# Performance work log

Hardware: AMD Instinct MI355X
Metric: run time of the kernel (lower is better)

The kernel has to match this reference:

```python
import jax, jax.numpy as jnp
import numpy as np

N = 50000
E = 1600000
IN_C = 128
HID = 64
HEADS = 4
OUT_C = 64
NEG_SLOPE = 0.2


def gat_layer(x, src, dst, W, a_src, a_dst, b, heads, ch):
    # x: [N, F_in], W: [F_in, heads*ch], a_src/a_dst: [heads, ch], b: [heads*ch]
    n = x.shape[0]
    h = (x @ W).reshape(n, heads, ch)                       # [N, H, C]
    alpha_s = jnp.einsum('nhc,hc->nh', h, a_src)            # [N, H]
    alpha_d = jnp.einsum('nhc,hc->nh', h, a_dst)
    e = jax.nn.leaky_relu(alpha_s[src] + alpha_d[dst], NEG_SLOPE)  # [Et, H]
    # segment softmax over incoming edges of each dst node (self-loops guarantee non-empty)
    m = jax.ops.segment_max(e, dst, num_segments=n)
    ex = jnp.exp(e - m[dst])
    denom = jax.ops.segment_sum(ex, dst, num_segments=n)
    alpha = ex / (denom[dst] + 1e-16)                       # [Et, H]
    out = jax.ops.segment_sum(h[src] * alpha[:, :, None], dst, num_segments=n)  # [N,H,C]
    return out.reshape(n, heads * ch) + b


def setup_inputs() -> dict:
    key = jax.random.key(0)
    ks = jax.random.split(key, 10)
    x = jax.random.normal(ks[0], (N, IN_C), dtype=jnp.float32)
    edge_index = jax.random.randint(ks[1], (2, E), 0, N, dtype=jnp.int64)
    s = 0.1
    W1 = jax.random.normal(ks[2], (IN_C, HEADS * HID), dtype=jnp.float32) * s
    a_src1 = jax.random.normal(ks[3], (HEADS, HID), dtype=jnp.float32) * s
    a_dst1 = jax.random.normal(ks[4], (HEADS, HID), dtype=jnp.float32) * s
    b1 = jnp.zeros((HEADS * HID,), dtype=jnp.float32)
    W2 = jax.random.normal(ks[5], (HEADS * HID, OUT_C), dtype=jnp.float32) * s
    a_src2 = jax.random.normal(ks[6], (1, OUT_C), dtype=jnp.float32) * s
    a_dst2 = jax.random.normal(ks[7], (1, OUT_C), dtype=jnp.float32) * s
    b2 = jnp.zeros((OUT_C,), dtype=jnp.float32)
    return {"x": x, "edge_index": edge_index, "W1": W1, "a_src1": a_src1,
            "a_dst1": a_dst1, "b1": b1, "W2": W2, "a_src2": a_src2,
            "a_dst2": a_dst2, "b2": b2}


def reference(x, edge_index, W1, a_src1, a_dst1, b1, W2, a_src2, a_dst2, b2):
    # add self-loops (PyG GATConv default)
    loops = jnp.arange(N, dtype=edge_index.dtype)
    src = jnp.concatenate([edge_index[0], loops])
    dst = jnp.concatenate([edge_index[1], loops])
    h = gat_layer(x, src, dst, W1, a_src1, a_dst1, b1, HEADS, HID)
    h = jax.nn.relu(h)
    out = gat_layer(h, src, dst, W2, a_src2, a_dst2, b2, 1, OUT_C)
    return out
```

## Files before the change

### kernel.cpp

```cpp
#include <hip/hip_runtime.h>
#include <cstdint>
#include <cstddef>

#define IN_C 128
#define CAP 72

typedef _Float16 __attribute__((ext_vector_type(2))) half2v;
typedef _Float16 __attribute__((ext_vector_type(4))) half4v;
typedef _Float16 __attribute__((ext_vector_type(8))) f16x8;
typedef float    __attribute__((ext_vector_type(4))) f32x4;
typedef unsigned __attribute__((ext_vector_type(2))) u32x2;
typedef unsigned __attribute__((ext_vector_type(4))) u32x4;

static __device__ __forceinline__ float lrelu(float x) { return x > 0.f ? x : 0.2f * x; }

static __device__ __forceinline__ unsigned pack2h(float a, float b) {
  union { _Float16 h[2]; unsigned u; } c;
  c.h[0] = (_Float16)a; c.h[1] = (_Float16)b;
  return c.u;
}
static __device__ __forceinline__ half2v bc_h2(unsigned u) {
  union { unsigned u; half2v h; } c; c.u = u; return c.h;
}

#if __has_builtin(__builtin_amdgcn_fdot2)
static __device__ __forceinline__ float FDOT2(half2v a, half2v b, float c) {
  return __builtin_amdgcn_fdot2(a, b, c, false);
}
#else
static __device__ __forceinline__ float FDOT2(half2v a, half2v b, float c) {
  return c + (float)a.x * (float)b.x + (float)a.y * (float)b.y;
}
#endif

__global__ void k_scatter_cnt(const int* __restrict__ ei_src, const int* __restrict__ ei_dst,
                              int* __restrict__ cnt, u32x2* __restrict__ sd,
                              int E, int Et, int nPerReg, int n) {
  int r = blockIdx.x & 7;
  int base = (blockIdx.x >> 3) * 1024 + threadIdx.x;
  int lo = r * nPerReg;
  int hi = lo + nPerReg; if (hi > n) hi = n;
#pragma unroll
  for (int k = 0; k < 4; ++k) {
    int e = base + k * 256;
    if (e >= Et) continue;
    int d = (e < E) ? __builtin_nontemporal_load(&ei_dst[e]) : (e - E);
    if (d < lo || d >= hi) continue;
    int s = (e < E) ? __builtin_nontemporal_load(&ei_src[e]) : d;
    int pos = atomicAdd(&cnt[d], 1);
    if (pos < CAP) {
      u32x2 rec = {(unsigned)s, (unsigned)d};
      sd[(size_t)d * CAP + pos] = rec;
    }
  }
}

__global__ void k_edgew(const u32x2* __restrict__ sd, const int* __restrict__ cnt,
                        const float* __restrict__ as1, const float* __restrict__ ad1,
                        u32x4* __restrict__ recs, int total) {
  int i = blockIdx.x * 256 + threadIdx.x;
  if (i >= total) return;
  int node = (int)((unsigned)i / CAP);
  int slot = i - node * CAP;
  int c = cnt[node]; if (c > CAP) c = CAP;
  if (slot >= c) return;
  u32x2 p = sd[i];
  float4 a = *(const float4*)&as1[p.x * 4];
  float4 b = *(const float4*)&ad1[p.y * 4];
  unsigned w01 = pack2h(__expf(lrelu(a.x + b.x)), __expf(lrelu(a.y + b.y)));
  unsigned w23 = pack2h(__expf(lrelu(a.z + b.z)), __expf(lrelu(a.w + b.w)));
  u32x4 rec = {p.x, w01, w23, p.y};
  recs[i] = rec;
}

__global__ void k_prep(const float* __restrict__ x, const float* __restrict__ W1,
                       const float* __restrict__ W2, const float* __restrict__ as_,
                       const float* __restrict__ ad_, _Float16* __restrict__ xh,
                       _Float16* __restrict__ W1t, _Float16* __restrict__ W2t,
                       float* __restrict__ V, int n4, int xb, int wb) {
  int b = blockIdx.x;
  if (b < xb) {
    int i = b * 256 + threadIdx.x;
    if (i >= n4) return;
    f32x4 v = __builtin_nontemporal_load((const f32x4*)&x[i * 4]);
    half4v o;
    o.x = (_Float16)v.x; o.y = (_Float16)v.y; o.z = (_Float16)v.z; o.w = (_Float16)v.w;
    *(half4v*)&xh[i * 4] = o;
  } else if (b < xb + wb) {
    int i = (b - xb) * 256 + threadIdx.x;
    if (i < 128 * 256) {
      int k = i / 256, nn = i % 256;
      W1t[(size_t)nn * 128 + k] = (_Float16)W1[i];
    } else {
      int j = i - 128 * 256;
      if (j < 256 * 64) {
        int k = j / 64, nn = j % 64;
        W2t[(size_t)nn * 256 + k] = (_Float16)W2[j];
      }
    }
  } else {
    int t = (b - xb - wb) * 256 + threadIdx.x;
    if (t >= 1024) return;
    int h = t >> 7, k = t & 127;
    int hh = h & 3;
    const float* av = (h < 4) ? as_ : ad_;
    float s = 0.f;
#pragma unroll 8
    for (int c = 0; c < 64; ++c) s += W1[k * 256 + hh * 64 + c] * av[hh * 64 + c];
    V[h * 128 + k] = s;
  }
}

__launch_bounds__(256)
__global__ void k_alpha1x(const _Float16* __restrict__ xh, const float* __restrict__ V,
                          float* __restrict__ as1, float* __restrict__ ad1, int n) {
  __shared__ float Vs[1024];
  int tid = threadIdx.x;
  for (int i = tid; i < 1024; i += 256) Vs[i] = V[i];
  __syncthreads();
  int wave = tid >> 6, lane = tid & 63;
  int node = blockIdx.x * 4 + wave;
  if (node >= n) return;
  half2v hv = *(const half2v*)&xh[(size_t)node * 128 + lane * 2];
  float x0 = (float)hv.x, x1 = (float)hv.y;
  float r[8];
#pragma unroll
  for (int h = 0; h < 8; ++h)
    r[h] = x0 * Vs[h * 128 + lane * 2] + x1 * Vs[h * 128 + lane * 2 + 1];
#pragma unroll
  for (int off = 1; off < 64; off <<= 1) {
#pragma unroll
    for (int h = 0; h < 8; ++h) r[h] += __shfl_xor(r[h], off);
  }
  if (lane == 0) {
#pragma unroll
    for (int h = 0; h < 4; ++h) {
      as1[node * 4 + h] = r[h];
      ad1[node * 4 + h] = r[4 + h];
    }
  }
}

__launch_bounds__(256)
__global__ void k_aggr1x(const int* __restrict__ cnt, const u32x4* __restrict__ recs,
                         const _Float16* __restrict__ xh, _Float16* __restrict__ agg, int n) {
  int wave = threadIdx.x >> 6, lane = threadIdx.x & 63;
  int node = blockIdx.x * 4 + wave;
  if (node >= n) return;
  int deg = cnt[node]; if (deg > CAP) deg = CAP;
  int beg = node * CAP, end = beg + deg;
  int g = lane >> 5, l32 = lane & 31;
  int ch0 = l32 * 4;
  const half2v ONE2 = bc_h2(0x3C003C00u);
  float acc[4][4] = {};
  float ds[4] = {};
  for (int i = beg; i < end; i += 8) {
    int i0 = i + (g << 1), i1 = i0 + 1, i2 = i0 + 4, i3 = i1 + 4;
    unsigned a0 = 0, a1 = 0, b0 = 0, b1 = 0;
    unsigned c0 = 0, c1 = 0, d0 = 0, d1 = 0;
    int s0 = 0, s1 = 0, s2 = 0, s3 = 0;
    if (i0 < end) { u32x4 r = recs[i0]; s0 = (int)r.x; a0 = r.y; a1 = r.z; }
    if (i1 < end) { u32x4 r = recs[i1]; s1 = (int)r.x; b0 = r.y; b1 = r.z; }
    if (i2 < end) { u32x4 r = recs[i2]; s2 = (int)r.x; c0 = r.y; c1 = r.z; }
    if (i3 < end) { u32x4 r = recs[i3]; s3 = (int)r.x; d0 = r.y; d1 = r.z; }
    u32x2 xa = *(const u32x2*)&xh[(size_t)s0 * 128 + ch0];
    u32x2 xb = *(const u32x2*)&xh[(size_t)s1 * 128 + ch0];
    u32x2 xc = *(const u32x2*)&xh[(size_t)s2 * 128 + ch0];
    u32x2 xd = *(const u32x2*)&xh[(size_t)s3 * 128 + ch0];
    {
      half2v P0 = bc_h2((a0 & 0xffffu) | (b0 << 16));
      half2v P1 = bc_h2((a0 >> 16) | (b0 & 0xffff0000u));
      half2v P2 = bc_h2((a1 & 0xffffu) | (b1 << 16));
      half2v P3 = bc_h2((a1 >> 16) | (b1 & 0xffff0000u));
      half2v Q0 = bc_h2((xa.x & 0xffffu) | (xb.x << 16));
      half2v Q1 = bc_h2((xa.x >> 16) | (xb.x & 0xffff0000u));
      half2v Q2 = bc_h2((xa.y & 0xffffu) | (xb.y << 16));
      half2v Q3 = bc_h2((xa.y >> 16) | (xb.y & 0xffff0000u));
      ds[0] = FDOT2(P0, ONE2, ds[0]); ds[1] = FDOT2(P1, ONE2, ds[1]);
      ds[2] = FDOT2(P2, ONE2, ds[2]); ds[3] = FDOT2(P3, ONE2, ds[3]);
      acc[0][0] = FDOT2(P0, Q0, acc[0][0]); acc[0][1] = FDOT2(P0, Q1, acc[0][1]);
      acc[0][2] = FDOT2(P0, Q2, acc[0][2]); acc[0][3] = FDOT2(P0, Q3, acc[0][3]);
      acc[1][0] = FDOT2(P1, Q0, acc[1][0]); acc[1][1] = FDOT2(P1, Q1, acc[1][1]);
      acc[1][2] = FDOT2(P1, Q2, acc[1][2]); acc[1][3] = FDOT2(P1, Q3, acc[1][3]);
      acc[2][0] = FDOT2(P2, Q0, acc[2][0]); acc[2][1] = FDOT2(P2, Q1, acc[2][1]);
      acc[2][2] = FDOT2(P2, Q2, acc[2][2]); acc[2][3] = FDOT2(P2, Q3, acc[2][3]);
      acc[3][0] = FDOT2(P3, Q0, acc[3][0]); acc[3][1] = FDOT2(P3, Q1, acc[3][1]);
      acc[3][2] = FDOT2(P3, Q2, acc[3][2]); acc[3][3] = FDOT2(P3, Q3, acc[3][3]);
    }
    {
      half2v P0 = bc_h2((c0 & 0xffffu) | (d0 << 16));
      half2v P1 = bc_h2((c0 >> 16) | (d0 & 0xffff0000u));
      half2v P2 = bc_h2((c1 & 0xffffu) | (d1 << 16));
      half2v P3 = bc_h2((c1 >> 16) | (d1 & 0xffff0000u));
      half2v Q0 = bc_h2((xc.x & 0xffffu) | (xd.x << 16));
      half2v Q1 = bc_h2((xc.x >> 16) | (xd.x & 0xffff0000u));
      half2v Q2 = bc_h2((xc.y & 0xffffu) | (xd.y << 16));
      half2v Q3 = bc_h2((xc.y >> 16) | (xd.y & 0xffff0000u));
      ds[0] = FDOT2(P0, ONE2, ds[0]); ds[1] = FDOT2(P1, ONE2, ds[1]);
      ds[2] = FDOT2(P2, ONE2, ds[2]); ds[3] = FDOT2(P3, ONE2, ds[3]);
      acc[0][0] = FDOT2(P0, Q0, acc[0][0]); acc[0][1] = FDOT2(P0, Q1, acc[0][1]);
      acc[0][2] = FDOT2(P0, Q2, acc[0][2]); acc[0][3] = FDOT2(P0, Q3, acc[0][3]);
      acc[1][0] = FDOT2(P1, Q0, acc[1][0]); acc[1][1] = FDOT2(P1, Q1, acc[1][1]);
      acc[1][2] = FDOT2(P1, Q2, acc[1][2]); acc[1][3] = FDOT2(P1, Q3, acc[1][3]);
      acc[2][0] = FDOT2(P2, Q0, acc[2][0]); acc[2][1] = FDOT2(P2, Q1, acc[2][1]);
      acc[2][2] = FDOT2(P2, Q2, acc[2][2]); acc[2][3] = FDOT2(P2, Q3, acc[2][3]);
      acc[3][0] = FDOT2(P3, Q0, acc[3][0]); acc[3][1] = FDOT2(P3, Q1, acc[3][1]);
      acc[3][2] = FDOT2(P3, Q2, acc[3][2]); acc[3][3] = FDOT2(P3, Q3, acc[3][3]);
    }
  }
#pragma unroll
  for (int h = 0; h < 4; ++h) {
    ds[h] += __shfl_xor(ds[h], 32);
#pragma unroll
    for (int j = 0; j < 4; ++j) acc[h][j] += __shfl_xor(acc[h][j], 32);
  }
  if (g == 0) {
#pragma unroll
    for (int h = 0; h < 4; ++h) {
      float inv = 1.0f / (ds[h] + 1e-16f);
      half4v o;
      o.x = (_Float16)(acc[h][0] * inv);
      o.y = (_Float16)(acc[h][1] * inv);
      o.z = (_Float16)(acc[h][2] * inv);
      o.w = (_Float16)(acc[h][3] * inv);
      *(half4v*)&agg[(size_t)node * 512 + h * 128 + ch0] = o;
    }
  }
}

__launch_bounds__(256)
__global__ void k_gemm1b(const _Float16* __restrict__ agg, const _Float16* __restrict__ W1t,
                         const float* __restrict__ b1, _Float16* __restrict__ hrelu, int M) {
  int w = threadIdx.x >> 6, lane = threadIdx.x & 63;
  int r = lane & 15, kg = lane >> 4;
  int m0 = blockIdx.x * 64 + w * 16;
  f32x4 acc[16];
#pragma unroll
  for (int c = 0; c < 16; ++c) acc[c] = (f32x4){0.f, 0.f, 0.f, 0.f};
  int mA = m0 + r; if (mA > M - 1) mA = M - 1;
  const _Float16* Arow = agg + (size_t)mA * 512 + kg * 8;
#pragma unroll
  for (int k0 = 0; k0 < 128; k0 += 32) {
    f16x8 a[4];
#pragma unroll
    for (int h = 0; h < 4; ++h) a[h] = *(const f16x8*)(Arow + h * 128 + k0);
#pragma unroll
    for (int c = 0; c < 16; ++c) {
      f16x8 b = *(const f16x8*)&W1t[(size_t)(c * 16 + r) * 128 + k0 + kg * 8];
      acc[c] = __builtin_amdgcn_mfma_f32_16x16x32_f16(a[c >> 2], b, acc[c], 0, 0, 0);
    }
  }
#pragma unroll
  for (int c = 0; c < 16; ++c) {
    float bv = b1[c * 16 + r];
#pragma unroll
    for (int j = 0; j < 4; ++j) {
      int m = m0 + kg * 4 + j;
      if (m < M) hrelu[(size_t)m * 256 + c * 16 + r] = (_Float16)fmaxf(acc[c][j] + bv, 0.f);
    }
  }
}

__launch_bounds__(256)
__global__ void k_gemm2_a(const _Float16* __restrict__ A, const _Float16* __restrict__ Bt,
                          const float* __restrict__ a_s, const float* __restrict__ a_d,
                          _Float16* __restrict__ C, float* __restrict__ as2,
                          float* __restrict__ ad2, int M) {
  int w = threadIdx.x >> 6, lane = threadIdx.x & 63;
  int r = lane & 15, kg = lane >> 4;
  int m0 = blockIdx.x * 64 + w * 16;
  f32x4 acc[4];
#pragma unroll
  for (int c = 0; c < 4; ++c) acc[c] = (f32x4){0.f, 0.f, 0.f, 0.f};
  int mA = m0 + r; if (mA > M - 1) mA = M - 1;
  const _Float16* Arow = A + (size_t)mA * 256 + kg * 8;
#pragma unroll
  for (int k0 = 0; k0 < 256; k0 += 32) {
    f16x8 a = *(const f16x8*)(Arow + k0);
#pragma unroll
    for (int c = 0; c < 4; ++c) {
      f16x8 b = *(const f16x8*)&Bt[(size_t)(c * 16 + r) * 256 + k0 + kg * 8];
      acc[c] = __builtin_amdgcn_mfma_f32_16x16x32_f16(a, b, acc[c], 0, 0, 0);
    }
  }
  float sp[4] = {}, dp[4] = {};
#pragma unroll
  for (int c = 0; c < 4; ++c) {
    float asv = a_s[c * 16 + r];
    float adv = a_d[c * 16 + r];
#pragma unroll
    for (int j = 0; j < 4; ++j) {
      float v = acc[c][j];
      sp[j] += v * asv;
      dp[j] += v * adv;
    }
  }
#pragma unroll
  for (int off = 1; off < 16; off <<= 1) {
#pragma unroll
    for (int j = 0; j < 4; ++j) {
      sp[j] += __shfl_xor(sp[j], off);
      dp[j] += __shfl_xor(dp[j], off);
    }
  }
#pragma unroll
  for (int c = 0; c < 4; ++c) {
#pragma unroll
    for (int j = 0; j < 4; ++j) {
      int m = m0 + kg * 4 + j;
      if (m < M) C[(size_t)m * 64 + c * 16 + r] = (_Float16)acc[c][j];
    }
  }
  if (r == 0) {
#pragma unroll
    for (int j = 0; j < 4; ++j) {
      int m = m0 + kg * 4 + j;
      if (m < M) { as2[m] = sp[j]; ad2[m] = dp[j]; }
    }
  }
}

__launch_bounds__(256)
__global__ void k_aggr2(const int* __restrict__ cnt, const u32x4* __restrict__ recs,
                        const float* __restrict__ as2, const float* __restrict__ ad2,
                        const _Float16* __restrict__ h2h, const float* __restrict__ b2,
                        float* __restrict__ out, int n) {
  int wave = threadIdx.x >> 6, lane = threadIdx.x & 63;
  int node = blockIdx.x * 4 + wave;
  if (node >= n) return;
  int deg = cnt[node]; if (deg > CAP) deg = CAP;
  int beg = node * CAP, end = beg + deg;
  float adm = ad2[node];
  int g = lane >> 4, l16 = lane & 15;
  int ch0 = l16 * 4;
  float acc[4] = {};
  float dsum = 0.f;
  for (int i = beg; i < end; i += 4) {
    int idx = i + g;
    int s = 0; float w = 0.f;
    if (idx < end) {
      s = (int)recs[idx].x;
      w = __expf(lrelu(as2[s] + adm));
    }
    half4v hv = *(const half4v*)&h2h[(size_t)s * 64 + ch0];
    dsum += w;
    acc[0] += w * (float)hv.x; acc[1] += w * (float)hv.y;
    acc[2] += w * (float)hv.z; acc[3] += w * (float)hv.w;
  }
#pragma unroll
  for (int off = 16; off < 64; off <<= 1) {
    dsum += __shfl_xor(dsum, off);
#pragma unroll
    for (int j = 0; j < 4; ++j) acc[j] += __shfl_xor(acc[j], off);
  }
  if (g == 0) {
    float inv = 1.0f / (dsum + 1e-16f);
    float4 o;
    o.x = acc[0] * inv + b2[ch0];
    o.y = acc[1] * inv + b2[ch0 + 1];
    o.z = acc[2] * inv + b2[ch0 + 2];
    o.w = acc[3] * inv + b2[ch0 + 3];
    *(float4*)&out[(size_t)node * 64 + ch0] = o;
  }
}

extern "C" void kernel_launch(void* const* d_in, const int* in_sizes, int n_in,
                              void* d_out, int out_size, void* d_ws, size_t ws_size,
                              hipStream_t stream) {
  const float* x    = (const float*)d_in[0];
  const int*   ei   = (const int*)d_in[1];
  const float* W1   = (const float*)d_in[2];
  const float* a_s1 = (const float*)d_in[3];
  const float* a_d1 = (const float*)d_in[4];
  const float* b1   = (const float*)d_in[5];
  const float* W2   = (const float*)d_in[6];
  const float* a_s2 = (const float*)d_in[7];
  const float* a_d2 = (const float*)d_in[8];
  const float* b2   = (const float*)d_in[9];
  float* out = (float*)d_out;

  const int n  = in_sizes[0] / IN_C;
  const int E  = in_sizes[1] / 2;
  const int Et = E + n;
  const int* ei_src = ei;
  const int* ei_dst = ei + E;

  char* ws = (char*)d_ws;
  size_t off = 0;
  auto alloc = [&](size_t bytes) -> void* {
    void* p = ws + off;
    off = (off + bytes + 255) & ~(size_t)255;
    return p;
  };
  _Float16* xh      = (_Float16*)alloc((size_t)n * 128 * 2);
  _Float16* W1t     = (_Float16*)alloc((size_t)256 * 128 * 2);
  _Float16* W2t     = (_Float16*)alloc((size_t)64 * 256 * 2);
  float*    V       = (float*)alloc((size_t)1024 * 4);
  _Float16* agg     = (_Float16*)alloc((size_t)n * 512 * 2);
  _Float16* hrelu_h = (_Float16*)alloc((size_t)n * 256 * 2);
  _Float16* h2h     = (_Float16*)alloc((size_t)n * 64 * 2);
  float* as1        = (float*)alloc((size_t)n * 4 * 4);
  float* ad1        = (float*)alloc((size_t)n * 4 * 4);
  float* as2        = (float*)alloc((size_t)n * 4);
  float* ad2        = (float*)alloc((size_t)n * 4);
  int* cnt          = (int*)alloc((size_t)n * 4);
  u32x2* sd         = (u32x2*)alloc((size_t)n * CAP * 8);
  u32x4* recs       = (u32x4*)alloc((size_t)n * CAP * 16);

  int nw  = (n + 3) / 4;
  int gx1 = (n + 63) / 64;
  int nPerReg = (n + 7) / 8;
  int n4  = n * 128 / 4;
  int xb  = (n4 + 255) / 256;
  int wb  = (128 * 256 + 256 * 64 + 255) / 256;
  int sb  = (Et + 1023) / 1024;
  int total = n * CAP;
  int tb  = (total + 255) / 256;

  (void)hipMemsetAsync(cnt, 0, (size_t)n * 4, stream);
  hipLaunchKernelGGL(k_scatter_cnt, dim3(sb * 8), dim3(256), 0, stream,
                     ei_src, ei_dst, cnt, sd, E, Et, nPerReg, n);

  hipLaunchKernelGGL(k_prep, dim3(xb + wb + 4), dim3(256), 0, stream,
                     x, W1, W2, a_s1, a_d1, xh, W1t, W2t, V, n4, xb, wb);
  hipLaunchKernelGGL(k_alpha1x, dim3(nw), dim3(256), 0, stream, xh, V, as1, ad1, n);

  hipLaunchKernelGGL(k_edgew, dim3(tb), dim3(256), 0, stream, sd, cnt, as1, ad1, recs, total);
  hipLaunchKernelGGL(k_aggr1x, dim3(nw), dim3(256), 0, stream, cnt, recs, xh, agg, n);
  hipLaunchKernelGGL(k_gemm1b, dim3(gx1), dim3(256), 0, stream, agg, W1t, b1, hrelu_h, n);

  hipLaunchKernelGGL(k_gemm2_a, dim3(gx1), dim3(256), 0, stream,
                     hrelu_h, W2t, a_s2, a_d2, h2h, as2, ad2, n);
  hipLaunchKernelGGL(k_aggr2, dim3(nw), dim3(256), 0, stream,
                     cnt, recs, as2, ad2, h2h, b2, out, n);
}
```

Measured before the change: 372.5 us.

## Store layer-1 edge weights pre-paired and precompute layer-2 edge weights separately

Layer-1 edge weights are now written in pair-interleaved form (two edges per record, half2 per head) with a separate source-index pair array. This removes the per-edge repacking shuffles in the aggregation kernel and cuts record bytes. Layer-2 edge exponentials are moved out of the aggregation loop into a new per-edge kernel that stores (src, weight), so aggr2 no longer does a dependent gather of as2 before its feature gather. The cost is an extra kernel launch and an extra pass over the edge list in memory.

```diff
diff --git a/kernel.cpp b/kernel.cpp
--- a/kernel.cpp
+++ b/kernel.cpp
@@ -4,6 +4,7 @@
 
 #define IN_C 128
 #define CAP 72
+#define PCAP 36
 
 typedef _Float16 __attribute__((ext_vector_type(2))) half2v;
 typedef _Float16 __attribute__((ext_vector_type(4))) half4v;
@@ -57,7 +58,36 @@
 
 __global__ void k_edgew(const u32x2* __restrict__ sd, const int* __restrict__ cnt,
                         const float* __restrict__ as1, const float* __restrict__ ad1,
-                        u32x4* __restrict__ recs, int total) {
+                        u32x2* __restrict__ spair, u32x4* __restrict__ wpair, int ptotal) {
+  int i = blockIdx.x * 256 + threadIdx.x;
+  if (i >= ptotal) return;
+  int node = (int)((unsigned)i / PCAP);
+  int p = i - node * PCAP;
+  int c = cnt[node]; if (c > CAP) c = CAP;
+  int npair = (c + 1) >> 1;
+  if (p >= npair) return;
+  u32x2 e0 = sd[(size_t)node * CAP + 2 * p];
+  bool has1 = (2 * p + 1) < c;
+  u32x2 e1 = has1 ? sd[(size_t)node * CAP + 2 * p + 1] : e0;
+  float4 bd = *(const float4*)&ad1[(size_t)e0.y * 4];
+  float4 a0 = *(const float4*)&as1[(size_t)e0.x * 4];
+  float4 a1 = *(const float4*)&as1[(size_t)e1.x * 4];
+  float A0 = __expf(lrelu(a0.x + bd.x)), A1 = __expf(lrelu(a0.y + bd.y));
+  float A2 = __expf(lrelu(a0.z + bd.z)), A3 = __expf(lrelu(a0.w + bd.w));
+  float B0 = 0.f, B1 = 0.f, B2 = 0.f, B3 = 0.f;
+  if (has1) {
+    B0 = __expf(lrelu(a1.x + bd.x)); B1 = __expf(lrelu(a1.y + bd.y));
+    B2 = __expf(lrelu(a1.z + bd.z)); B3 = __expf(lrelu(a1.w + bd.w));
+  }
+  u32x4 wp = {pack2h(A0, B0), pack2h(A1, B1), pack2h(A2, B2), pack2h(A3, B3)};
+  u32x2 sp = {e0.x, e1.x};
+  wpair[i] = wp;
+  spair[i] = sp;
+}
+
+__global__ void k_edgew2(const u32x2* __restrict__ sd, const int* __restrict__ cnt,
+                         const float* __restrict__ as2, const float* __restrict__ ad2,
+                         u32x2* __restrict__ sw2, int total) {
   int i = blockIdx.x * 256 + threadIdx.x;
   if (i >= total) return;
   int node = (int)((unsigned)i / CAP);
@@ -65,12 +95,10 @@
   int c = cnt[node]; if (c > CAP) c = CAP;
   if (slot >= c) return;
   u32x2 p = sd[i];
-  float4 a = *(const float4*)&as1[p.x * 4];
-  float4 b = *(const float4*)&ad1[p.y * 4];
-  unsigned w01 = pack2h(__expf(lrelu(a.x + b.x)), __expf(lrelu(a.y + b.y)));
-  unsigned w23 = pack2h(__expf(lrelu(a.z + b.z)), __expf(lrelu(a.w + b.w)));
-  u32x4 rec = {p.x, w01, w23, p.y};
-  recs[i] = rec;
+  float w = __expf(lrelu(as2[p.x] + ad2[p.y]));
+  union { float f; unsigned u; } cv; cv.f = w;
+  u32x2 o = {p.x, cv.u};
+  sw2[i] = o;
 }
 
 __global__ void k_prep(const float* __restrict__ x, const float* __restrict__ W1,
@@ -142,36 +170,34 @@
 }
 
 __launch_bounds__(256)
-__global__ void k_aggr1x(const int* __restrict__ cnt, const u32x4* __restrict__ recs,
-                         const _Float16* __restrict__ xh, _Float16* __restrict__ agg, int n) {
+__global__ void k_aggr1x(const int* __restrict__ cnt, const u32x2* __restrict__ spair,
+                         const u32x4* __restrict__ wpair, const _Float16* __restrict__ xh,
+                         _Float16* __restrict__ agg, int n) {
   int wave = threadIdx.x >> 6, lane = threadIdx.x & 63;
   int node = blockIdx.x * 4 + wave;
   if (node >= n) return;
   int deg = cnt[node]; if (deg > CAP) deg = CAP;
-  int beg = node * CAP, end = beg + deg;
+  int npair = (deg + 1) >> 1;
+  int base = node * PCAP;
   int g = lane >> 5, l32 = lane & 31;
   int ch0 = l32 * 4;
   const half2v ONE2 = bc_h2(0x3C003C00u);
   float acc[4][4] = {};
   float ds[4] = {};
-  for (int i = beg; i < end; i += 8) {
-    int i0 = i + (g << 1), i1 = i0 + 1, i2 = i0 + 4, i3 = i1 + 4;
-    unsigned a0 = 0, a1 = 0, b0 = 0, b1 = 0;
-    unsigned c0 = 0, c1 = 0, d0 = 0, d1 = 0;
-    int s0 = 0, s1 = 0, s2 = 0, s3 = 0;
-    if (i0 < end) { u32x4 r = recs[i0]; s0 = (int)r.x; a0 = r.y; a1 = r.z; }
-    if (i1 < end) { u32x4 r = recs[i1]; s1 = (int)r.x; b0 = r.y; b1 = r.z; }
-    if (i2 < end) { u32x4 r = recs[i2]; s2 = (int)r.x; c0 = r.y; c1 = r.z; }
-    if (i3 < end) { u32x4 r = recs[i3]; s3 = (int)r.x; d0 = r.y; d1 = r.z; }
+  for (int p0 = 0; p0 < npair; p0 += 4) {
+    int pA = base + p0 + g;
+    int pB = pA + 2;
+    int lim = base + npair;
+    unsigned s0 = 0, s1 = 0, s2 = 0, s3 = 0;
+    u32x4 wA = {0, 0, 0, 0}, wB = {0, 0, 0, 0};
+    if (pA < lim) { u32x2 sp = spair[pA]; s0 = sp.x; s1 = sp.y; wA = wpair[pA]; }
+    if (pB < lim) { u32x2 sp = spair[pB]; s2 = sp.x; s3 = sp.y; wB = wpair[pB]; }
     u32x2 xa = *(const u32x2*)&xh[(size_t)s0 * 128 + ch0];
     u32x2 xb = *(const u32x2*)&xh[(size_t)s1 * 128 + ch0];
     u32x2 xc = *(const u32x2*)&xh[(size_t)s2 * 128 + ch0];
     u32x2 xd = *(const u32x2*)&xh[(size_t)s3 * 128 + ch0];
     {
-      half2v P0 = bc_h2((a0 & 0xffffu) | (b0 << 16));
-      half2v P1 = bc_h2((a0 >> 16) | (b0 & 0xffff0000u));
-      half2v P2 = bc_h2((a1 & 0xffffu) | (b1 << 16));
-      half2v P3 = bc_h2((a1 >> 16) | (b1 & 0xffff0000u));
+      half2v P0 = bc_h2(wA.x), P1 = bc_h2(wA.y), P2 = bc_h2(wA.z), P3 = bc_h2(wA.w);
       half2v Q0 = bc_h2((xa.x & 0xffffu) | (xb.x << 16));
       half2v Q1 = bc_h2((xa.x >> 16) | (xb.x & 0xffff0000u));
       half2v Q2 = bc_h2((xa.y & 0xffffu) | (xb.y << 16));
@@ -188,10 +214,7 @@
       acc[3][2] = FDOT2(P3, Q2, acc[3][2]); acc[3][3] = FDOT2(P3, Q3, acc[3][3]);
     }
     {
-      half2v P0 = bc_h2((c0 & 0xffffu) | (d0 << 16));
-      half2v P1 = bc_h2((c0 >> 16) | (d0 & 0xffff0000u));
-      half2v P2 = bc_h2((c1 & 0xffffu) | (d1 << 16));
-      half2v P3 = bc_h2((c1 >> 16) | (d1 & 0xffff0000u));
+      half2v P0 = bc_h2(wB.x), P1 = bc_h2(wB.y), P2 = bc_h2(wB.z), P3 = bc_h2(wB.w);
       half2v Q0 = bc_h2((xc.x & 0xffffu) | (xd.x << 16));
       half2v Q1 = bc_h2((xc.x >> 16) | (xd.x & 0xffff0000u));
       half2v Q2 = bc_h2((xc.y & 0xffffu) | (xd.y << 16));
@@ -321,8 +344,7 @@
 }
 
 __launch_bounds__(256)
-__global__ void k_aggr2(const int* __restrict__ cnt, const u32x4* __restrict__ recs,
-                        const float* __restrict__ as2, const float* __restrict__ ad2,
+__global__ void k_aggr2(const int* __restrict__ cnt, const u32x2* __restrict__ sw2,
                         const _Float16* __restrict__ h2h, const float* __restrict__ b2,
                         float* __restrict__ out, int n) {
   int wave = threadIdx.x >> 6, lane = threadIdx.x & 63;
@@ -330,7 +352,6 @@
   if (node >= n) return;
   int deg = cnt[node]; if (deg > CAP) deg = CAP;
   int beg = node * CAP, end = beg + deg;
-  float adm = ad2[node];
   int g = lane >> 4, l16 = lane & 15;
   int ch0 = l16 * 4;
   float acc[4] = {};
@@ -339,8 +360,9 @@
     int idx = i + g;
     int s = 0; float w = 0.f;
     if (idx < end) {
-      s = (int)recs[idx].x;
-      w = __expf(lrelu(as2[s] + adm));
+      u32x2 r = sw2[idx];
+      s = (int)r.x;
+      union { unsigned u; float f; } c; c.u = r.y; w = c.f;
     }
     half4v hv = *(const half4v*)&h2h[(size_t)s * 64 + ch0];
     dsum += w;
@@ -405,7 +427,9 @@
   float* ad2        = (float*)alloc((size_t)n * 4);
   int* cnt          = (int*)alloc((size_t)n * 4);
   u32x2* sd         = (u32x2*)alloc((size_t)n * CAP * 8);
-  u32x4* recs       = (u32x4*)alloc((size_t)n * CAP * 16);
+  u32x2* spair      = (u32x2*)alloc((size_t)n * PCAP * 8);
+  u32x4* wpair      = (u32x4*)alloc((size_t)n * PCAP * 16);
+  u32x2* sw2        = (u32x2*)alloc((size_t)n * CAP * 8);
 
   int nw  = (n + 3) / 4;
   int gx1 = (n + 63) / 64;
@@ -414,8 +438,10 @@
   int xb  = (n4 + 255) / 256;
   int wb  = (128 * 256 + 256 * 64 + 255) / 256;
   int sb  = (Et + 1023) / 1024;
-  int total = n * CAP;
+  int total  = n * CAP;
+  int ptotal = n * PCAP;
   int tb  = (total + 255) / 256;
+  int pb  = (ptotal + 255) / 256;
 
   (void)hipMemsetAsync(cnt, 0, (size_t)n * 4, stream);
   hipLaunchKernelGGL(k_scatter_cnt, dim3(sb * 8), dim3(256), 0, stream,
@@ -425,12 +451,12 @@
                      x, W1, W2, a_s1, a_d1, xh, W1t, W2t, V, n4, xb, wb);
   hipLaunchKernelGGL(k_alpha1x, dim3(nw), dim3(256), 0, stream, xh, V, as1, ad1, n);
 
-  hipLaunchKernelGGL(k_edgew, dim3(tb), dim3(256), 0, stream, sd, cnt, as1, ad1, recs, total);
-  hipLaunchKernelGGL(k_aggr1x, dim3(nw), dim3(256), 0, stream, cnt, recs, xh, agg, n);
+  hipLaunchKernelGGL(k_edgew, dim3(pb), dim3(256), 0, stream, sd, cnt, as1, ad1, spair, wpair, ptotal);
+  hipLaunchKernelGGL(k_aggr1x, dim3(nw), dim3(256), 0, stream, cnt, spair, wpair, xh, agg, n);
   hipLaunchKernelGGL(k_gemm1b, dim3(gx1), dim3(256), 0, stream, agg, W1t, b1, hrelu_h, n);
 
   hipLaunchKernelGGL(k_gemm2_a, dim3(gx1), dim3(256), 0, stream,
                      hrelu_h, W2t, a_s2, a_d2, h2h, as2, ad2, n);
-  hipLaunchKernelGGL(k_aggr2, dim3(nw), dim3(256), 0, stream,
-                     cnt, recs, as2, ad2, h2h, b2, out, n);
-}
+  hipLaunchKernelGGL(k_edgew2, dim3(tb), dim3(256), 0, stream, sd, cnt, as2, ad2, sw2, total);
+  hipLaunchKernelGGL(k_aggr2, dim3(nw), dim3(256), 0, stream, cnt, sw2, h2h, b2, out, n);
+}
```

New measurement: 354.9 us. 4.7% less time.
